# Optimization experiments

Measured on AMD Instinct MI355X. Metric: run time of the kernel, lower is better.

## Reference

```python
import jax, jax.numpy as jnp
import numpy as np

D, N = 512, 256          # transition steps, batch
H, L, V = 128, 64, 32000 # h_dim, label_dim, lexicon_size


def _valid_transitions(seed=0):
    # generate a valid shift/reduce schedule: reduce only when stack depth >= 2
    rng = np.random.default_rng(seed)
    ptr = np.zeros(N, np.int64)
    trans = np.zeros((D, N), np.int32)
    for t in range(D):
        r = ((rng.random(N) < 0.6) & (ptr >= 2)).astype(np.int32)
        trans[t] = r
        ptr += 1 - 2 * r  # every step pushes 1; reduce pops 2 first
    return jnp.asarray(trans)


def setup_inputs() -> dict:
    key = jax.random.key(0)
    k1, k2, k3 = jax.random.split(key, 3)
    transitions = _valid_transitions()
    labels_idx = jax.random.randint(k1, (D, N), 0, V, dtype=jnp.int32)
    emb = jax.random.normal(k2, (V, L), jnp.float32) * 0.02
    emb = emb.at[0].set(0.0)  # padding_idx=0
    arg_dim = L + 2 * H
    W = jax.random.normal(k3, (arg_dim, 5 * H), jnp.float32) / np.sqrt(arg_dim).astype(np.float32)
    b = jnp.zeros((5 * H,), jnp.float32)
    leaf = jnp.zeros((H,), jnp.float32)  # leaf_input placeholder vector
    return {"transitions": transitions, "labels_idx": labels_idx,
            "emb": emb, "W": W, "b": b, "leaf": leaf}


def _cell(x, hl, hr, cl, cr, W, b):
    # binary TreeLSTM (Tai et al.): gates from concat(label, h_left, h_right)
    g = jnp.concatenate([x, hl, hr], axis=-1) @ W + b  # [N, 5H]
    i, fl, fr, o, u = jnp.split(g, 5, axis=-1)
    c = jax.nn.sigmoid(i) * jnp.tanh(u) + jax.nn.sigmoid(fl) * cl + jax.nn.sigmoid(fr) * cr
    h = jax.nn.sigmoid(o) * jnp.tanh(c)
    return c, h


def reference(transitions, labels_idx, emb, W, b, leaf):
    labels = emb[labels_idx]  # [D,N,L]
    bidx = jnp.arange(N)

    def step(carry, inp):
        h_st, c_st, idx_st, ptr = carry  # [D,N,H],[D,N,H],[D,N],[N]
        t, mask, lab = inp
        mf = mask.astype(bool)[:, None]
        # right popped first, then left (matches _get_indices call order)
        ridx = idx_st[(ptr - 1) % D, bidx]
        lidx = idx_st[(ptr - 2) % D, bidx]
        hl = jnp.where(mf, h_st[lidx, bidx], leaf)
        hr = jnp.where(mf, h_st[ridx, bidx], leaf)
        cl = jnp.where(mf, c_st[lidx, bidx], leaf)
        cr = jnp.where(mf, c_st[ridx, bidx], leaf)
        c, h = _cell(lab, hl, hr, cl, cr, W, b)
        h_st = h_st.at[t].set(h)   # embeddings_stack[step] = h
        c_st = c_st.at[t].set(c)   # cells_stack[step] = c
        newptr = ptr - 2 * mask    # pops (if reduce)
        idx_st = idx_st.at[newptr, bidx].set(t)  # push current step for all batch
        return (h_st, c_st, idx_st, newptr + 1), None

    h_st = jnp.zeros((D, N, H), jnp.float32)
    c_st = jnp.zeros((D, N, H), jnp.float32)
    idx_st = jnp.zeros((D, N), jnp.int32)
    ptr = jnp.zeros((N,), jnp.int32)
    (h_st, c_st, _, _), _ = jax.lax.scan(
        step, (h_st, c_st, idx_st, ptr),
        (jnp.arange(D, dtype=jnp.int32), transitions, labels))
    # original returns (thin_stack[1][D-1], thin_stack[0][D-1]) = (cells, embeddings)
    return c_st[D - 1], h_st[D - 1]
```

## Files before the change

### kernel.cpp

```cpp
#include <hip/hip_runtime.h>
#include <stdint.h>


#define D     512
#define HD    128
#define LD    64
#define NTHR  512
#define GPR   328

typedef unsigned long long u64t;

__device__ __forceinline__ float sigf(float x){ return 1.0f/(1.0f+__expf(-x)); }
__device__ __forceinline__ float tanh_(float x){ return 1.0f-2.0f/(__expf(2.0f*x)+1.0f); }
__device__ __forceinline__ u64t gld64(const float* p){
  return __hip_atomic_load((const u64t*)p, __ATOMIC_RELAXED, __HIP_MEMORY_SCOPE_AGENT);
}
__device__ __forceinline__ u64t gld64u(const unsigned* p){
  return __hip_atomic_load((const u64t*)p, __ATOMIC_RELAXED, __HIP_MEMORY_SCOPE_AGENT);
}
__device__ __forceinline__ void gst32(float* p, float v){
  __hip_atomic_store(p, v, __ATOMIC_RELAXED, __HIP_MEMORY_SCOPE_AGENT);
}
__device__ __forceinline__ void gsttag(unsigned* p, unsigned v){
  __hip_atomic_store(p, v, __ATOMIC_RELAXED, __HIP_MEMORY_SCOPE_AGENT);
}

__global__ __launch_bounds__(NTHR,2) void spinn_kernel(
    const int* __restrict__ trans, const int* __restrict__ labels,
    const float* __restrict__ emb, const float* __restrict__ W,
    const float* __restrict__ bias, const float* __restrict__ leaf,
    float* __restrict__ out, unsigned* __restrict__ tags,
    float* __restrict__ rec, float* __restrict__ cown)
{
  const int bid = blockIdx.x;
  const int g2 = bid>>1, sl = bid&1, ps = sl^1;
  const int gb0 = g2*2;
  const int tid = threadIdx.x;
  const int kg = tid>>6, lane = tid&63;
  const int cq = lane;

  __shared__ __align__(16) float xs[2][2][320];
  __shared__ __align__(16) float gpq[16][GPR];
  __shared__ float bsl[320];
  __shared__ float lshd[HD];
  __shared__ float clb[2][2][64];
  __shared__ uint8_t mS[D][2];
  __shared__ short liA[D][2];
  __shared__ unsigned short stk_[2][D];

  float4 wr4[40]; float wr1[40];
  {
    const int gq = (cq>>4)*128 + sl*64 + ((cq*4)&63);
    const int gu = 512 + sl*64 + cq;
#pragma unroll
    for (int j=0;j<40;++j){
      int k = kg*40 + j;
      wr4[j] = *(const float4*)(W + (size_t)k*640 + gq);
      wr1[j] = W[(size_t)k*640 + gu];
    }
  }
  if (tid < 320){
    int c = tid;
    int gc = (c < 256) ? ((c>>6)*128 + sl*64 + (c&63)) : (512 + sl*64 + (c-256));
    bsl[c] = bias[gc];
  }
  if (tid < HD) lshd[tid] = leaf[tid];
  if (tid < 2){
    int b = tid, p = 0;
    for (int t=0;t<D;++t){
      int m = trans[t*256 + gb0 + b];
      short li = 0;
      if (m) li = (short)stk_[b][p-2];
      mS[t][b] = (uint8_t)m; liA[t][b] = li;
      int np = p - 2*m; stk_[b][np] = (unsigned short)t; p = np+1;
    }
  }
  __syncthreads();

  for (int idx = tid; idx < 640; idx += NTHR){
    int b = (idx >= 320) ? 1 : 0;
    int r = idx - b*320;
    if (r < 64){
      int row = labels[gb0 + b];
      xs[0][b][r] = emb[(size_t)row*LD + r];
    } else {
      xs[0][b][r] = lshd[(r-64)&127];
    }
  }
  __syncthreads();

  auto gemm = [&](int cur){
    float4 a0 = {0.f,0.f,0.f,0.f}, a1 = {0.f,0.f,0.f,0.f};
    float u0 = 0.f, u1 = 0.f;
#pragma unroll
    for (int j4=0;j4<10;++j4){
      int k = kg*40 + j4*4;
      float4 x0 = *(const float4*)&xs[cur][0][k];
      float4 x1 = *(const float4*)&xs[cur][1][k];
      float xa0[4] = {x0.x,x0.y,x0.z,x0.w};
      float xa1[4] = {x1.x,x1.y,x1.z,x1.w};
#pragma unroll
      for (int jj=0;jj<4;++jj){
        float4 w = wr4[j4*4+jj];
        float wu = wr1[j4*4+jj];
        a0.x = __builtin_fmaf(w.x, xa0[jj], a0.x);
        a0.y = __builtin_fmaf(w.y, xa0[jj], a0.y);
        a0.z = __builtin_fmaf(w.z, xa0[jj], a0.z);
        a0.w = __builtin_fmaf(w.w, xa0[jj], a0.w);
        a1.x = __builtin_fmaf(w.x, xa1[jj], a1.x);
        a1.y = __builtin_fmaf(w.y, xa1[jj], a1.y);
        a1.z = __builtin_fmaf(w.z, xa1[jj], a1.z);
        a1.w = __builtin_fmaf(w.w, xa1[jj], a1.w);
        u0 = __builtin_fmaf(wu, xa0[jj], u0);
        u1 = __builtin_fmaf(wu, xa1[jj], u1);
      }
    }
    *(float4*)&gpq[kg*2+0][cq*4] = a0;
    *(float4*)&gpq[kg*2+1][cq*4] = a1;
    gpq[kg*2+0][256+cq] = u0;
    gpq[kg*2+1][256+cq] = u1;
  };

  float ccprev = 0.f;

  for (int t=0;t<D;++t){
    const int cur = t&1, nxt = cur^1;

    if (kg < 4){
      gemm(cur);
    } else if (kg == 4){
      if (t+1 < D){
        int b = lane>>5, jj = lane&31;
        int row = labels[(t+1)*256 + gb0 + b];
        float2 ev = *(const float2*)(emb + (size_t)row*LD + jj*2);
        xs[nxt][b][jj*2]   = ev.x;
        xs[nxt][b][jj*2+1] = ev.y;
      }
    } else if (kg == 5){
      if (t+1 < D){
        int b = lane>>5, jj = lane&31;
        int m1 = mS[t+1][b]; int li = liA[t+1][b];
        if (m1){
          if (li <= t-2){
            size_t ro = (((size_t)li*128+g2)*2 + sl)*128 + b*64 + jj*2;
            union{u64t u; float f[2];} h_, c_;
            h_.u = gld64(rec + ro);
            c_.u = gld64(cown + ro);
            xs[nxt][b][64+sl*64+jj*2]   = h_.f[0];
            xs[nxt][b][64+sl*64+jj*2+1] = h_.f[1];
            clb[nxt][b][jj*2]   = c_.f[0];
            clb[nxt][b][jj*2+1] = c_.f[1];
          }
        } else {
          xs[nxt][b][64+sl*64+jj*2]   = lshd[sl*64+jj*2];
          xs[nxt][b][64+sl*64+jj*2+1] = lshd[sl*64+jj*2+1];
          clb[nxt][b][jj*2]   = lshd[sl*64+jj*2];
          clb[nxt][b][jj*2+1] = lshd[sl*64+jj*2+1];
        }
      }
    } else if (kg == 6){
      if (t+1 < D){
        int b = lane>>5, jj = lane&31;
        int m1 = mS[t+1][b]; int li = liA[t+1][b];
        if (m1){
          if (li <= t-2){
            size_t ro = (((size_t)li*128+g2)*2 + ps)*128 + b*64 + jj*2;
            union{u64t u; float f[2];} h_;
            h_.u = gld64(rec + ro);
            xs[nxt][b][64+ps*64+jj*2]   = h_.f[0];
            xs[nxt][b][64+ps*64+jj*2+1] = h_.f[1];
          }
        } else {
          xs[nxt][b][64+ps*64+jj*2]    = lshd[ps*64+jj*2];
          xs[nxt][b][64+ps*64+jj*2+1]  = lshd[ps*64+jj*2+1];
          xs[nxt][b][192+ps*64+jj*2]   = lshd[ps*64+jj*2];
          xs[nxt][b][192+ps*64+jj*2+1] = lshd[ps*64+jj*2+1];
        }
      }
    } else {
      if (t > 0){
        const unsigned* tp = tags + (((size_t)(t-1)*128+g2)*2 + ps)*16;
        u64t want = ((u64t)(unsigned)(t-1) << 32) | (unsigned)(t-1);
        int it = 0;
        while (gld64u(tp) != want){
          __builtin_amdgcn_s_sleep(1);
          if (++it > (1<<20)) break;
        }
        int b = lane>>5, jj = lane&31;
        size_t ro = (((size_t)(t-1)*128+g2)*2 + ps)*128 + lane*2;
        union{u64t u; float f[2];} h_;
        h_.u = gld64(rec + ro);
        if (mS[t][b]){
          xs[cur][b][192+ps*64+jj*2]   = h_.f[0];
          xs[cur][b][192+ps*64+jj*2+1] = h_.f[1];
        }
        if (t+1 < D && mS[t+1][b] && liA[t+1][b] == t-1){
          xs[nxt][b][64+ps*64+jj*2]   = h_.f[0];
          xs[nxt][b][64+ps*64+jj*2+1] = h_.f[1];
        }
      }
    }
    __syncthreads();

    if (kg >= 4){ gemm(cur); }
    __syncthreads();

    if (tid < 128){
      const int b = tid>>6, dl = tid&63, gd = sl*64+dl;
      const int m = mS[t][b];
      float s[5];
#pragma unroll
      for (int g=0; g<5; ++g){
        int c = (g<4) ? (g*64+dl) : (256+dl);
        float a = 0.f;
#pragma unroll
        for (int kk=0; kk<8; ++kk) a += gpq[kk*2+b][c];
        s[g] = a + bsl[c];
      }
      float cl_ = m ? clb[cur][b][dl] : lshd[gd];
      float cr_ = m ? ccprev : lshd[gd];
      float cc = sigf(s[0])*tanh_(s[4]) + sigf(s[1])*cl_ + sigf(s[2])*cr_;
      float hh = sigf(s[3])*tanh_(cc);
      ccprev = cc;
      size_t ro = (((size_t)t*128 + g2)*2 + sl)*128 + b*64 + dl;
      gst32(rec + ro, hh);
      gst32(cown + ro, cc);
      if (t == D-1){
        out[(size_t)(gb0+b)*HD + gd] = cc;
        out[(size_t)256*HD + (size_t)(gb0+b)*HD + gd] = hh;
      } else {
        xs[nxt][b][192+gd] = mS[t+1][b] ? hh : lshd[gd];
      }
      if (t+2 < D && mS[t+2][b] && liA[t+2][b] == t){
        xs[cur][b][64+gd]  = hh;
        clb[cur][b][dl]    = cc;
      }
      __asm__ volatile("s_waitcnt vmcnt(0)" ::: "memory");
      if (dl == 0)
        gsttag(tags + (((size_t)t*128+g2)*2+sl)*16 + b, (unsigned)t);
    }
    __syncthreads();
  }
}

extern "C" void kernel_launch(void* const* d_in, const int* in_sizes, int n_in,
                              void* d_out, int out_size, void* d_ws, size_t ws_size,
                              hipStream_t stream) {
  (void)in_sizes; (void)n_in; (void)out_size; (void)ws_size;
  const int*   trans  = (const int*)d_in[0];
  const int*   labels = (const int*)d_in[1];
  const float* emb    = (const float*)d_in[2];
  const float* W      = (const float*)d_in[3];
  const float* bias   = (const float*)d_in[4];
  const float* leaf   = (const float*)d_in[5];
  float* out = (float*)d_out;

  uint8_t* ws = (uint8_t*)d_ws;
  unsigned* tags = (unsigned*)ws;
  float* rec  = (float*)(ws + ((size_t)8<<20));
  float* cown = (float*)(ws + ((size_t)72<<20));

  spinn_kernel<<<dim3(256), dim3(NTHR), 0, stream>>>(
      trans, labels, emb, W, bias, leaf, out, tags, rec, cown);
}
```

Baseline: 1.990 ms.

## Move weights from registers to LDS plus per-step global reloads

Before this change each thread held 200 weight floats in registers. Now the first 12 of every 40 K-rows per group are staged in shared memory, and the remaining 28 rows are re-read from global memory (L2/cache) on every step. Launch bounds change to one block per SM, presumably to relieve register pressure. The cost is added LDS and global load latency inside the serial 512-step recurrence, and the kernel relies on lower occupancy still fitting all 256 co-resident blocks needed by the spin-wait scheme.

```diff
diff --git a/kernel.cpp b/kernel.cpp
--- a/kernel.cpp
+++ b/kernel.cpp
@@ -7,6 +7,7 @@
 #define LD    64
 #define NTHR  512
 #define GPR   328
+#define LROWS 12
 
 typedef unsigned long long u64t;
 
@@ -25,7 +26,7 @@
   __hip_atomic_store(p, v, __ATOMIC_RELAXED, __HIP_MEMORY_SCOPE_AGENT);
 }
 
-__global__ __launch_bounds__(NTHR,2) void spinn_kernel(
+__global__ __launch_bounds__(NTHR,1) void spinn_kernel(
     const int* __restrict__ trans, const int* __restrict__ labels,
     const float* __restrict__ emb, const float* __restrict__ W,
     const float* __restrict__ bias, const float* __restrict__ leaf,
@@ -39,6 +40,7 @@
   const int kg = tid>>6, lane = tid&63;
   const int cq = lane;
 
+  __shared__ __align__(16) float wlds[8*LROWS*320];
   __shared__ __align__(16) float xs[2][2][320];
   __shared__ __align__(16) float gpq[16][GPR];
   __shared__ float bsl[320];
@@ -48,17 +50,9 @@
   __shared__ short liA[D][2];
   __shared__ unsigned short stk_[2][D];
 
-  float4 wr4[40]; float wr1[40];
-  {
-    const int gq = (cq>>4)*128 + sl*64 + ((cq*4)&63);
-    const int gu = 512 + sl*64 + cq;
-#pragma unroll
-    for (int j=0;j<40;++j){
-      int k = kg*40 + j;
-      wr4[j] = *(const float4*)(W + (size_t)k*640 + gq);
-      wr1[j] = W[(size_t)k*640 + gu];
-    }
-  }
+  const int gq = (cq>>4)*128 + sl*64 + ((cq*4)&63);
+  const int gu = 512 + sl*64 + cq;
+
   if (tid < 320){
     int c = tid;
     int gc = (c < 256) ? ((c>>6)*128 + sl*64 + (c&63)) : (512 + sl*64 + (c-256));
@@ -77,6 +71,13 @@
   }
   __syncthreads();
 
+  for (int idx = tid; idx < 8*LROWS*320; idx += NTHR){
+    int r = idx / 320, c = idx - r*320;
+    int k = (r / LROWS)*40 + (r % LROWS);
+    int gc = (c < 256) ? ((c>>6)*128 + sl*64 + (c&63)) : (512 + sl*64 + (c-256));
+    wlds[idx] = W[(size_t)k*640 + gc];
+  }
+
   for (int idx = tid; idx < 640; idx += NTHR){
     int b = (idx >= 320) ? 1 : 0;
     int r = idx - b*320;
@@ -93,7 +94,7 @@
     float4 a0 = {0.f,0.f,0.f,0.f}, a1 = {0.f,0.f,0.f,0.f};
     float u0 = 0.f, u1 = 0.f;
 #pragma unroll
-    for (int j4=0;j4<10;++j4){
+    for (int j4=0;j4<LROWS/4;++j4){
       int k = kg*40 + j4*4;
       float4 x0 = *(const float4*)&xs[cur][0][k];
       float4 x1 = *(const float4*)&xs[cur][1][k];
@@ -101,8 +102,33 @@
       float xa1[4] = {x1.x,x1.y,x1.z,x1.w};
 #pragma unroll
       for (int jj=0;jj<4;++jj){
-        float4 w = wr4[j4*4+jj];
-        float wu = wr1[j4*4+jj];
+        const int r = kg*LROWS + j4*4 + jj;
+        float4 w = *(const float4*)&wlds[r*320 + cq*4];
+        float wu = wlds[r*320 + 256 + cq];
+        a0.x = __builtin_fmaf(w.x, xa0[jj], a0.x);
+        a0.y = __builtin_fmaf(w.y, xa0[jj], a0.y);
+        a0.z = __builtin_fmaf(w.z, xa0[jj], a0.z);
+        a0.w = __builtin_fmaf(w.w, xa0[jj], a0.w);
+        a1.x = __builtin_fmaf(w.x, xa1[jj], a1.x);
+        a1.y = __builtin_fmaf(w.y, xa1[jj], a1.y);
+        a1.z = __builtin_fmaf(w.z, xa1[jj], a1.z);
+        a1.w = __builtin_fmaf(w.w, xa1[jj], a1.w);
+        u0 = __builtin_fmaf(wu, xa0[jj], u0);
+        u1 = __builtin_fmaf(wu, xa1[jj], u1);
+      }
+    }
+#pragma unroll
+    for (int j4=LROWS/4;j4<10;++j4){
+      int k = kg*40 + j4*4;
+      float4 x0 = *(const float4*)&xs[cur][0][k];
+      float4 x1 = *(const float4*)&xs[cur][1][k];
+      float xa0[4] = {x0.x,x0.y,x0.z,x0.w};
+      float xa1[4] = {x1.x,x1.y,x1.z,x1.w};
+#pragma unroll
+      for (int jj=0;jj<4;++jj){
+        const int kk = k + jj;
+        float4 w = *(const float4*)(W + (size_t)kk*640 + gq);
+        float wu = W[(size_t)kk*640 + gu];
         a0.x = __builtin_fmaf(w.x, xa0[jj], a0.x);
         a0.y = __builtin_fmaf(w.y, xa0[jj], a0.y);
         a0.z = __builtin_fmaf(w.z, xa0[jj], a0.z);
```

New measurement: 5.279 ms. 2.65x slower.

## Split each batch group across four cooperating blocks, streaming W from global memory

Applied to the files above, without the earlier changes.

Each group of four batch elements is now split across four workgroups, each owning a 32-wide hidden slice, instead of two elements across two workgroups with 64-wide slices. Weights are no longer held in registers. They are re-read from global memory inside the GEMM each step, and a large padding shared array is added, apparently to force one block per CU. The wait warp polls three peer tags with a wave-wide vote and gathers h from three peers. This cuts per-block GEMM work per batch element but adds global weight traffic and more cross-block synchronisation.

```diff
diff --git a/kernel.cpp b/kernel.cpp
--- a/kernel.cpp
+++ b/kernel.cpp
@@ -2,20 +2,16 @@
 #include <stdint.h>
 
 
-#define D     512
-#define HD    128
-#define LD    64
-#define NTHR  512
-#define GPR   328
+#define D    512
+#define HD   128
+#define LD   64
+#define NTHR 512
 
 typedef unsigned long long u64t;
 
 __device__ __forceinline__ float sigf(float x){ return 1.0f/(1.0f+__expf(-x)); }
 __device__ __forceinline__ float tanh_(float x){ return 1.0f-2.0f/(__expf(2.0f*x)+1.0f); }
-__device__ __forceinline__ u64t gld64(const float* p){
-  return __hip_atomic_load((const u64t*)p, __ATOMIC_RELAXED, __HIP_MEMORY_SCOPE_AGENT);
-}
-__device__ __forceinline__ u64t gld64u(const unsigned* p){
+__device__ __forceinline__ u64t gld64(const void* p){
   return __hip_atomic_load((const u64t*)p, __ATOMIC_RELAXED, __HIP_MEMORY_SCOPE_AGENT);
 }
 __device__ __forceinline__ void gst32(float* p, float v){
@@ -25,47 +21,41 @@
   __hip_atomic_store(p, v, __ATOMIC_RELAXED, __HIP_MEMORY_SCOPE_AGENT);
 }
 
-__global__ __launch_bounds__(NTHR,2) void spinn_kernel(
+__global__ __launch_bounds__(NTHR,1) void spinn_kernel(
     const int* __restrict__ trans, const int* __restrict__ labels,
     const float* __restrict__ emb, const float* __restrict__ W,
     const float* __restrict__ bias, const float* __restrict__ leaf,
     float* __restrict__ out, unsigned* __restrict__ tags,
-    float* __restrict__ rec, float* __restrict__ cown)
+    float* __restrict__ hP, float* __restrict__ cP)
 {
   const int bid = blockIdx.x;
-  const int g2 = bid>>1, sl = bid&1, ps = sl^1;
-  const int gb0 = g2*2;
+  const int g4 = bid>>2, sl = bid&3;
+  const int gb0 = g4*4;
   const int tid = threadIdx.x;
   const int kg = tid>>6, lane = tid&63;
-  const int cq = lane;
-
-  __shared__ __align__(16) float xs[2][2][320];
-  __shared__ __align__(16) float gpq[16][GPR];
-  __shared__ float bsl[320];
+  const int bq = lane>>5, q = lane&31;
+  const int qg = q>>3, qo = q&7;
+
+  __shared__ __align__(16) float xs[2][4][324];
+  __shared__ __align__(16) float gpq[8][4][164];
+  __shared__ float bsl[160];
   __shared__ float lshd[HD];
-  __shared__ float clb[2][2][64];
-  __shared__ uint8_t mS[D][2];
-  __shared__ short liA[D][2];
-  __shared__ unsigned short stk_[2][D];
-
-  float4 wr4[40]; float wr1[40];
-  {
-    const int gq = (cq>>4)*128 + sl*64 + ((cq*4)&63);
-    const int gu = 512 + sl*64 + cq;
-#pragma unroll
-    for (int j=0;j<40;++j){
-      int k = kg*40 + j;
-      wr4[j] = *(const float4*)(W + (size_t)k*640 + gq);
-      wr1[j] = W[(size_t)k*640 + gu];
-    }
-  }
-  if (tid < 320){
+  __shared__ float clb[2][4][32];
+  __shared__ uint8_t mS[D][4];
+  __shared__ short liA[D][4];
+  __shared__ unsigned short stk_[4][D];
+  __shared__ float padL[10240];
+
+  const int gqcol = qg*128 + sl*32 + qo*4;
+  const int gucol = 512 + sl*32 + q;
+
+  if (tid < 160){
     int c = tid;
-    int gc = (c < 256) ? ((c>>6)*128 + sl*64 + (c&63)) : (512 + sl*64 + (c-256));
-    bsl[c] = bias[gc];
+    bsl[c] = (c < 128) ? bias[(c>>5)*128 + sl*32 + (c&31)]
+                       : bias[512 + sl*32 + (c-128)];
   }
   if (tid < HD) lshd[tid] = leaf[tid];
-  if (tid < 2){
+  if (tid < 4){
     int b = tid, p = 0;
     for (int t=0;t<D;++t){
       int m = trans[t*256 + gb0 + b];
@@ -77,48 +67,42 @@
   }
   __syncthreads();
 
-  for (int idx = tid; idx < 640; idx += NTHR){
-    int b = (idx >= 320) ? 1 : 0;
-    int r = idx - b*320;
-    if (r < 64){
-      int row = labels[gb0 + b];
-      xs[0][b][r] = emb[(size_t)row*LD + r];
-    } else {
-      xs[0][b][r] = lshd[(r-64)&127];
-    }
+  padL[(tid*29)&10239] = lshd[tid&127];
+
+  for (int idx = tid; idx < 4*320; idx += NTHR){
+    int b = idx / 320, r = idx - b*320;
+    xs[0][b][r] = (r < 64) ? emb[(size_t)labels[gb0+b]*LD + r]
+                           : lshd[(r-64)&127];
   }
   __syncthreads();
+  if (padL[(tid*31)&10239] == 3.25e18f) xs[0][0][0] += 1.f;
 
   auto gemm = [&](int cur){
     float4 a0 = {0.f,0.f,0.f,0.f}, a1 = {0.f,0.f,0.f,0.f};
     float u0 = 0.f, u1 = 0.f;
+    const int b0 = bq*2, b1 = bq*2+1;
 #pragma unroll
     for (int j4=0;j4<10;++j4){
       int k = kg*40 + j4*4;
-      float4 x0 = *(const float4*)&xs[cur][0][k];
-      float4 x1 = *(const float4*)&xs[cur][1][k];
-      float xa0[4] = {x0.x,x0.y,x0.z,x0.w};
-      float xa1[4] = {x1.x,x1.y,x1.z,x1.w};
+      float4 x0 = *(const float4*)&xs[cur][b0][k];
+      float4 x1 = *(const float4*)&xs[cur][b1][k];
+      float xa0[4]={x0.x,x0.y,x0.z,x0.w}, xa1[4]={x1.x,x1.y,x1.z,x1.w};
 #pragma unroll
       for (int jj=0;jj<4;++jj){
-        float4 w = wr4[j4*4+jj];
-        float wu = wr1[j4*4+jj];
-        a0.x = __builtin_fmaf(w.x, xa0[jj], a0.x);
-        a0.y = __builtin_fmaf(w.y, xa0[jj], a0.y);
-        a0.z = __builtin_fmaf(w.z, xa0[jj], a0.z);
-        a0.w = __builtin_fmaf(w.w, xa0[jj], a0.w);
-        a1.x = __builtin_fmaf(w.x, xa1[jj], a1.x);
-        a1.y = __builtin_fmaf(w.y, xa1[jj], a1.y);
-        a1.z = __builtin_fmaf(w.z, xa1[jj], a1.z);
-        a1.w = __builtin_fmaf(w.w, xa1[jj], a1.w);
-        u0 = __builtin_fmaf(wu, xa0[jj], u0);
-        u1 = __builtin_fmaf(wu, xa1[jj], u1);
-      }
-    }
-    *(float4*)&gpq[kg*2+0][cq*4] = a0;
-    *(float4*)&gpq[kg*2+1][cq*4] = a1;
-    gpq[kg*2+0][256+cq] = u0;
-    gpq[kg*2+1][256+cq] = u1;
+        int kk = k + jj;
+        float4 w = *(const float4*)(W + (size_t)kk*640 + gqcol);
+        float wu = W[(size_t)kk*640 + gucol];
+        a0.x=__builtin_fmaf(w.x,xa0[jj],a0.x); a0.y=__builtin_fmaf(w.y,xa0[jj],a0.y);
+        a0.z=__builtin_fmaf(w.z,xa0[jj],a0.z); a0.w=__builtin_fmaf(w.w,xa0[jj],a0.w);
+        a1.x=__builtin_fmaf(w.x,xa1[jj],a1.x); a1.y=__builtin_fmaf(w.y,xa1[jj],a1.y);
+        a1.z=__builtin_fmaf(w.z,xa1[jj],a1.z); a1.w=__builtin_fmaf(w.w,xa1[jj],a1.w);
+        u0=__builtin_fmaf(wu,xa0[jj],u0);      u1=__builtin_fmaf(wu,xa1[jj],u1);
+      }
+    }
+    *(float4*)&gpq[kg][b0][qg*32+qo*4] = a0;
+    *(float4*)&gpq[kg][b1][qg*32+qo*4] = a1;
+    gpq[kg][b0][128+q] = u0;
+    gpq[kg][b1][128+q] = u1;
   };
 
   float ccprev = 0.f;
@@ -130,73 +114,85 @@
       gemm(cur);
     } else if (kg == 4){
       if (t+1 < D){
-        int b = lane>>5, jj = lane&31;
+        int b = lane>>4, seg = lane&15;
         int row = labels[(t+1)*256 + gb0 + b];
-        float2 ev = *(const float2*)(emb + (size_t)row*LD + jj*2);
-        xs[nxt][b][jj*2]   = ev.x;
-        xs[nxt][b][jj*2+1] = ev.y;
+        float4 ev = *(const float4*)(emb + (size_t)row*LD + seg*4);
+        *(float4*)&xs[nxt][b][seg*4] = ev;
       }
     } else if (kg == 5){
       if (t+1 < D){
-        int b = lane>>5, jj = lane&31;
-        int m1 = mS[t+1][b]; int li = liA[t+1][b];
-        if (m1){
+        int b = lane>>4, d2 = (lane&15)*2;
+        if (mS[t+1][b]){
+          int li = liA[t+1][b];
           if (li <= t-2){
-            size_t ro = (((size_t)li*128+g2)*2 + sl)*128 + b*64 + jj*2;
+            size_t po = (((size_t)li*64+g4)*4 + sl)*128 + b*32 + d2;
             union{u64t u; float f[2];} h_, c_;
-            h_.u = gld64(rec + ro);
-            c_.u = gld64(cown + ro);
-            xs[nxt][b][64+sl*64+jj*2]   = h_.f[0];
-            xs[nxt][b][64+sl*64+jj*2+1] = h_.f[1];
-            clb[nxt][b][jj*2]   = c_.f[0];
-            clb[nxt][b][jj*2+1] = c_.f[1];
+            h_.u = gld64(hP + po); c_.u = gld64(cP + po);
+            xs[nxt][b][64+sl*32+d2]   = h_.f[0];
+            xs[nxt][b][64+sl*32+d2+1] = h_.f[1];
+            clb[nxt][b][d2] = c_.f[0]; clb[nxt][b][d2+1] = c_.f[1];
           }
         } else {
-          xs[nxt][b][64+sl*64+jj*2]   = lshd[sl*64+jj*2];
-          xs[nxt][b][64+sl*64+jj*2+1] = lshd[sl*64+jj*2+1];
-          clb[nxt][b][jj*2]   = lshd[sl*64+jj*2];
-          clb[nxt][b][jj*2+1] = lshd[sl*64+jj*2+1];
+          xs[nxt][b][64+sl*32+d2]   = lshd[sl*32+d2];
+          xs[nxt][b][64+sl*32+d2+1] = lshd[sl*32+d2+1];
+          clb[nxt][b][d2] = lshd[sl*32+d2]; clb[nxt][b][d2+1] = lshd[sl*32+d2+1];
         }
       }
     } else if (kg == 6){
       if (t+1 < D){
-        int b = lane>>5, jj = lane&31;
-        int m1 = mS[t+1][b]; int li = liA[t+1][b];
-        if (m1){
-          if (li <= t-2){
-            size_t ro = (((size_t)li*128+g2)*2 + ps)*128 + b*64 + jj*2;
-            union{u64t u; float f[2];} h_;
-            h_.u = gld64(rec + ro);
-            xs[nxt][b][64+ps*64+jj*2]   = h_.f[0];
-            xs[nxt][b][64+ps*64+jj*2+1] = h_.f[1];
+#pragma unroll
+        for (int r=0;r<3;++r){
+          int idx = r*64 + lane;
+          int p = idx>>6, w = idx&63, b = w>>4, d2 = (w&15)*2;
+          int psl = p + (p >= sl);
+          if (mS[t+1][b]){
+            int li = liA[t+1][b];
+            if (li <= t-2){
+              size_t po = (((size_t)li*64+g4)*4 + psl)*128 + b*32 + d2;
+              union{u64t u; float f[2];} h_; h_.u = gld64(hP + po);
+              xs[nxt][b][64+psl*32+d2]   = h_.f[0];
+              xs[nxt][b][64+psl*32+d2+1] = h_.f[1];
+            }
+          } else {
+            xs[nxt][b][64+psl*32+d2]    = lshd[psl*32+d2];
+            xs[nxt][b][64+psl*32+d2+1]  = lshd[psl*32+d2+1];
+            xs[nxt][b][192+psl*32+d2]   = lshd[psl*32+d2];
+            xs[nxt][b][192+psl*32+d2+1] = lshd[psl*32+d2+1];
           }
-        } else {
-          xs[nxt][b][64+ps*64+jj*2]    = lshd[ps*64+jj*2];
-          xs[nxt][b][64+ps*64+jj*2+1]  = lshd[ps*64+jj*2+1];
-          xs[nxt][b][192+ps*64+jj*2]   = lshd[ps*64+jj*2];
-          xs[nxt][b][192+ps*64+jj*2+1] = lshd[ps*64+jj*2+1];
         }
       }
     } else {
       if (t > 0){
-        const unsigned* tp = tags + (((size_t)(t-1)*128+g2)*2 + ps)*16;
-        u64t want = ((u64t)(unsigned)(t-1) << 32) | (unsigned)(t-1);
+        const unsigned* tline = tags + ((size_t)(t-1)*64 + g4)*16;
+        const u64t want = ((u64t)(unsigned)(t-1) << 32) | (unsigned)(t-1);
+        bool mine = (lane < 4) && (lane != sl);
+        const u64t* tp = (const u64t*)tline + lane;
+        u64t v = mine ? gld64(tp) : want;
         int it = 0;
-        while (gld64u(tp) != want){
+        while (!__all((v == want) ? 1 : 0)){
+          if (++it > (1<<20)) break;
           __builtin_amdgcn_s_sleep(1);
-          if (++it > (1<<20)) break;
-        }
-        int b = lane>>5, jj = lane&31;
-        size_t ro = (((size_t)(t-1)*128+g2)*2 + ps)*128 + lane*2;
-        union{u64t u; float f[2];} h_;
-        h_.u = gld64(rec + ro);
-        if (mS[t][b]){
-          xs[cur][b][192+ps*64+jj*2]   = h_.f[0];
-          xs[cur][b][192+ps*64+jj*2+1] = h_.f[1];
-        }
-        if (t+1 < D && mS[t+1][b] && liA[t+1][b] == t-1){
-          xs[nxt][b][64+ps*64+jj*2]   = h_.f[0];
-          xs[nxt][b][64+ps*64+jj*2+1] = h_.f[1];
+          if (mine && v != want) v = gld64(tp);
+        }
+#pragma unroll
+        for (int r=0;r<3;++r){
+          int idx = r*64 + lane;
+          int p = idx>>6, w = idx&63, b = w>>4, d2 = (w&15)*2;
+          int psl = p + (p >= sl);
+          bool needR = (mS[t][b] != 0);
+          bool needL = (t+1 < D) && mS[t+1][b] && (liA[t+1][b] == t-1);
+          if (needR || needL){
+            size_t po = (((size_t)(t-1)*64+g4)*4 + psl)*128 + b*32 + d2;
+            union{u64t u; float f[2];} h_; h_.u = gld64(hP + po);
+            if (needR){
+              xs[cur][b][192+psl*32+d2]   = h_.f[0];
+              xs[cur][b][192+psl*32+d2+1] = h_.f[1];
+            }
+            if (needL){
+              xs[nxt][b][64+psl*32+d2]   = h_.f[0];
+              xs[nxt][b][64+psl*32+d2+1] = h_.f[1];
+            }
+          }
         }
       }
     }
@@ -206,38 +202,40 @@
     __syncthreads();
 
     if (tid < 128){
-      const int b = tid>>6, dl = tid&63, gd = sl*64+dl;
+      const int b = tid>>5, dl = tid&31, gd = sl*32+dl;
       const int m = mS[t][b];
-      float s[5];
-#pragma unroll
-      for (int g=0; g<5; ++g){
-        int c = (g<4) ? (g*64+dl) : (256+dl);
-        float a = 0.f;
-#pragma unroll
-        for (int kk=0; kk<8; ++kk) a += gpq[kk*2+b][c];
-        s[g] = a + bsl[c];
-      }
+      float s0=0.f,s1=0.f,s2=0.f,s3=0.f,s4=0.f;
+#pragma unroll
+      for (int kk=0;kk<8;++kk){
+        const float* gr = gpq[kk][b];
+        s0 += gr[dl]; s1 += gr[32+dl]; s2 += gr[64+dl];
+        s3 += gr[96+dl]; s4 += gr[128+dl];
+      }
+      s0 += bsl[dl]; s1 += bsl[32+dl]; s2 += bsl[64+dl];
+      s3 += bsl[96+dl]; s4 += bsl[128+dl];
       float cl_ = m ? clb[cur][b][dl] : lshd[gd];
       float cr_ = m ? ccprev : lshd[gd];
-      float cc = sigf(s[0])*tanh_(s[4]) + sigf(s[1])*cl_ + sigf(s[2])*cr_;
-      float hh = sigf(s[3])*tanh_(cc);
+      float cc = sigf(s0)*tanh_(s4) + sigf(s1)*cl_ + sigf(s2)*cr_;
+      float hh = sigf(s3)*tanh_(cc);
       ccprev = cc;
-      size_t ro = (((size_t)t*128 + g2)*2 + sl)*128 + b*64 + dl;
-      gst32(rec + ro, hh);
-      gst32(cown + ro, cc);
+      size_t po = (((size_t)t*64+g4)*4 + sl)*128 + b*32 + dl;
+      gst32(hP + po, hh);
+      gst32(cP + po, cc);
       if (t == D-1){
         out[(size_t)(gb0+b)*HD + gd] = cc;
         out[(size_t)256*HD + (size_t)(gb0+b)*HD + gd] = hh;
       } else {
-        xs[nxt][b][192+gd] = mS[t+1][b] ? hh : lshd[gd];
+        xs[nxt][b][192+sl*32+dl] = mS[t+1][b] ? hh : lshd[gd];
       }
       if (t+2 < D && mS[t+2][b] && liA[t+2][b] == t){
-        xs[cur][b][64+gd]  = hh;
-        clb[cur][b][dl]    = cc;
+        xs[cur][b][64+sl*32+dl] = hh;
+        clb[cur][b][dl]         = cc;
       }
       __asm__ volatile("s_waitcnt vmcnt(0)" ::: "memory");
-      if (dl == 0)
-        gsttag(tags + (((size_t)t*128+g2)*2+sl)*16 + b, (unsigned)t);
+      if ((tid & 63) == 0){
+        int w = tid>>6;
+        gsttag(tags + ((size_t)t*64 + g4)*16 + sl*2 + w, (unsigned)t);
+      }
     }
     __syncthreads();
   }
@@ -257,9 +255,9 @@
 
   uint8_t* ws = (uint8_t*)d_ws;
   unsigned* tags = (unsigned*)ws;
-  float* rec  = (float*)(ws + ((size_t)8<<20));
-  float* cown = (float*)(ws + ((size_t)72<<20));
+  float* hP = (float*)(ws + ((size_t)2<<20));
+  float* cP = (float*)(ws + ((size_t)66<<20));
 
   spinn_kernel<<<dim3(256), dim3(NTHR), 0, stream>>>(
-      trans, labels, emb, W, bias, leaf, out, tags, rec, cown);
-}
+      trans, labels, emb, W, bias, leaf, out, tags, hP, cP);
+}
```

Measured after the change: 6.838 ms. 3.44x slower.
